# Performance work log

Measured on AMD Instinct MI355X. Metric: run time of the kernel, lower is better.

## Reference

```python
import jax, jax.numpy as jnp
import numpy as np

B, N, C = 16, 1024, 768
NUM_HEADS = 8
HEAD_DIM = C // NUM_HEADS
TEMP_INIT = 0.05
EPS_NORM = 1e-12   # F.normalize eps
EPS_LN = 1e-5      # LayerNorm eps


def setup_inputs() -> dict:
    key = jax.random.key(0)
    ks = jax.random.split(key, 4)
    x = jax.random.normal(ks[0], (B, N, C), dtype=jnp.float32)
    w_qkv = jax.random.normal(ks[1], (3 * C, C), dtype=jnp.float32) * (1.0 / np.sqrt(C))
    w_proj = jax.random.normal(ks[2], (C, C), dtype=jnp.float32) * (1.0 / np.sqrt(C))
    temperature = jnp.ones((NUM_HEADS, 1, 1), dtype=jnp.float32) * TEMP_INIT
    conv_w = jax.random.normal(ks[3], (C, 1, 3, 3), dtype=jnp.float32) * (1.0 / 3.0)
    gamma = jnp.ones((C,), dtype=jnp.float32)
    beta = jnp.zeros((C,), dtype=jnp.float32)
    return {"x": x, "w_qkv": w_qkv, "w_proj": w_proj, "temperature": temperature,
            "conv_w": conv_w, "gamma": gamma, "beta": beta, "H": 32, "W": 32}


def _l2norm_tokens(t):
    # normalize along token dim (axis=-2), matching F.normalize(dim=-2)
    n = jnp.sqrt(jnp.sum(t * t, axis=-2, keepdims=True))
    return t / jnp.maximum(n, EPS_NORM)


def reference(x, w_qkv, w_proj, temperature, conv_w, gamma, beta, H, W):
    b, n, c = x.shape
    h, d = NUM_HEADS, HEAD_DIM
    qkv = (x @ w_qkv.T).reshape(b, n, 3, h, d).transpose(2, 0, 3, 1, 4)  # [3,B,h,N,d]
    q, k, v = qkv[0], qkv[1], qkv[2]
    q = _l2norm_tokens(q)
    k = _l2norm_tokens(k)
    # cross-covariance attention over channels: [B,h,d,d]
    A = jnp.einsum('bhnd,bhne->bhde', q, k) / temperature[None]
    A = jax.nn.softmax(A, axis=-1)
    # v @ A^T : [B,h,N,d]
    x_xca = jnp.einsum('bhne,bhde->bhnd', v, A)
    x_xca = x_xca.transpose(0, 2, 1, 3).reshape(b, n, c)
    x_xca = x_xca @ w_proj.T
    # depthwise 3x3 local propagation
    x_img = x.transpose(0, 2, 1).reshape(b, c, H, W)
    x_local = jax.lax.conv_general_dilated(
        x_img, conv_w, window_strides=(1, 1), padding=((1, 1), (1, 1)),
        dimension_numbers=('NCHW', 'OIHW', 'NCHW'), feature_group_count=c)
    x_local = x_local.reshape(b, c, n).transpose(0, 2, 1)
    y = x_xca + 0.1 * x_local
    mu = jnp.mean(y, axis=-1, keepdims=True)
    var = jnp.mean((y - mu) ** 2, axis=-1, keepdims=True)
    return (y - mu) * jax.lax.rsqrt(var + EPS_LN) * gamma + beta
```

## Files before the change

### kernel.cpp

```cpp
#include <hip/hip_runtime.h>

#define DEVI __device__ __forceinline__

typedef __bf16 bf16x8 __attribute__((ext_vector_type(8)));
typedef float f32x4 __attribute__((ext_vector_type(4)));

DEVI unsigned short f2bf(float f) {
  unsigned u = __builtin_bit_cast(unsigned, f);
  u += 0x7FFFu + ((u >> 16) & 1u);
  return (unsigned short)(u >> 16);
}
DEVI float bf2f(unsigned short s) {
  return __builtin_bit_cast(float, ((unsigned)s) << 16);
}
DEVI f32x4 mfma16(bf16x8 a, bf16x8 b, f32x4 c) {
  return __builtin_amdgcn_mfma_f32_16x16x32_bf16(a, b, c, 0, 0, 0);
}
DEVI void gload16(const void* g, void* l) {
  __builtin_amdgcn_global_load_lds(
      (const __attribute__((address_space(1))) void*)g,
      (__attribute__((address_space(3))) void*)l, 16, 0, 0);
}
template <int ROWB>
DEVI bf16x8 frag_ld(const char* lds, int row, int kb) {
  int off = row * ROWB + (kb ^ ((row & 7) << 4));
  return __builtin_bit_cast(bf16x8, *(const uint4*)(lds + off));
}

__global__ __launch_bounds__(256) void k_cvt2(const float* __restrict__ a,
                                              unsigned short* __restrict__ oa, int n4a,
                                              const float* __restrict__ b,
                                              unsigned short* __restrict__ ob, int n4b) {
  const int tid = threadIdx.x;
  if (blockIdx.x < 2048) {
    const int chunk = (blockIdx.x & 7) * 256 + (blockIdx.x >> 3);
    const int i0 = chunk * 1536;
    for (int i = i0 + tid; i < i0 + 1536; i += 256) {
      float4 f = ((const float4*)a)[i];
      ushort4 o;
      o.x = f2bf(f.x); o.y = f2bf(f.y); o.z = f2bf(f.z); o.w = f2bf(f.w);
      ((ushort4*)oa)[i] = o;
    }
  } else {
    for (int i = (blockIdx.x - 2048) * 256 + tid; i < n4b; i += 256 * 256) {
      float4 f = ((const float4*)b)[i];
      ushort4 o;
      o.x = f2bf(f.x); o.y = f2bf(f.y); o.z = f2bf(f.z); o.w = f2bf(f.w);
      ((ushort4*)ob)[i] = o;
    }
  }
}

template <int MODE>
DEVI void gemm_body(char* lds, const unsigned short* __restrict__ A,
                    const unsigned short* __restrict__ B0,
                    unsigned short* __restrict__ o0, unsigned short* __restrict__ o1,
                    unsigned short* __restrict__ o2) {
  const int tid = threadIdx.x, l = tid & 63, wid = tid >> 6;
  const int wr = wid >> 2, wc = wid & 3;
  const int xg = blockIdx.x;
  const int CPX = MODE ? 64 : 192;
  const int NJT = MODE ? 4 : 12;
  const int li = (xg & 7) * CPX + (xg >> 3);
  const int jt = li % NJT, mt = li / NJT;
  const int m0 = mt * 128, j0 = jt * 192;
  const unsigned short* Bb = MODE ? B0 + (size_t)(m0 >> 10) * 589824 : B0;

  const unsigned short* srcg[4][2];
  int ldso[4][2];
#pragma unroll
  for (int sg = 0; sg < 4; ++sg) {
    const bool isA = (sg == 0) || (sg == 3);
#pragma unroll
    for (int i = 0; i < 2; ++i) {
      int c;
      if (sg == 0)      c = (wid < 4) ? wid : wid + 4;
      else if (sg == 3) c = (wid < 4) ? wid + 4 : wid + 8;
      else if (sg == 1) { int cc = 2 * wid + i; c = (cc >> 2) * 6 + (cc & 3); }
      else              c = (wid >> 1) * 6 + 4 + (wid & 1);
      const int r0 = 8 * c;
      const int r = r0 + (l >> 3);
      const int scol = ((l & 7) ^ (l >> 3)) << 3;
      srcg[sg][i] = (isA ? A + (size_t)(m0 + r) * 768 : Bb + (size_t)(j0 + r) * 768) + scol;
      ldso[sg][i] = (isA ? 0 : 16384) + r0 * 128;
    }
  }
  const int swz = (l & 7) << 4;
  const int uu = (l >> 4) << 4;
  const int c0 = uu ^ swz;
  const int c1 = (64 | uu) ^ swz;
  const int arow = (wr * 64 + (l & 15)) * 128;
  const int brow = 16384 + (wc * 48 + (l & 15)) * 128;

  f32x4 acc[4][3];
#pragma unroll
  for (int i = 0; i < 4; ++i)
#pragma unroll
    for (int j = 0; j < 3; ++j)
#pragma unroll
      for (int e = 0; e < 4; ++e) acc[i][j][e] = 0.f;
  bf16x8 a[2][2], a2[2][2], b01[2][2], b2[2];

#define STAGE1(sg, nxt, ko) \
  gload16(srcg[sg][0] + (ko), lds + (nxt)*40960 + ldso[sg][0])
#define STAGE2(sg, nxt, ko)                                        \
  do {                                                             \
    gload16(srcg[sg][0] + (ko), lds + (nxt)*40960 + ldso[sg][0]);  \
    gload16(srcg[sg][1] + (ko), lds + (nxt)*40960 + ldso[sg][1]);  \
  } while (0)
#define LD128(off) __builtin_bit_cast(bf16x8, *(const uint4*)(cb_ + (off)))

  STAGE1(0, 0, 0); STAGE2(1, 0, 0); STAGE1(2, 0, 0); STAGE1(3, 0, 0);
  asm volatile("s_waitcnt vmcnt(2)" ::: "memory");
  __builtin_amdgcn_s_barrier();

#define KBODY(KT, LASTF)                                                              \
  {                                                                                   \
    const char* cb_ = lds + ((KT) & 1) * 40960;                                       \
    const int nxt = (((KT) & 1) ^ 1);                                                 \
    const int ko = ((KT) + 1) * 64;                                                   \
                           \
    _Pragma("unroll") for (int mf = 0; mf < 2; ++mf) {                                \
      a[mf][0] = LD128(arow + mf * 2048 + c0);                                        \
      a[mf][1] = LD128(arow + mf * 2048 + c1);                                        \
    }                                                                                 \
    _Pragma("unroll") for (int nf = 0; nf < 2; ++nf) {                                \
      b01[nf][0] = LD128(brow + nf * 2048 + c0);                                      \
      b01[nf][1] = LD128(brow + nf * 2048 + c1);                                      \
    }                                                                                 \
    if (!(LASTF)) {                                                                   \
      STAGE1(0, nxt, ko); STAGE2(1, nxt, ko);                                         \
      asm volatile("s_waitcnt vmcnt(3)" ::: "memory");                                \
    } else {                                                                          \
      asm volatile("s_waitcnt vmcnt(0)" ::: "memory");                                \
    }                                                                                 \
    __builtin_amdgcn_s_barrier();                                                     \
    __builtin_amdgcn_s_setprio(1);                                                    \
    _Pragma("unroll") for (int mf = 0; mf < 2; ++mf)                                  \
      _Pragma("unroll") for (int nf = 0; nf < 2; ++nf) {                              \
        acc[mf][nf] = mfma16(a[mf][0], b01[nf][0], acc[mf][nf]);                      \
        acc[mf][nf] = mfma16(a[mf][1], b01[nf][1], acc[mf][nf]);                      \
      }                                                                               \
    __builtin_amdgcn_s_setprio(0);                                                    \
              \
    b2[0] = LD128(brow + 2 * 2048 + c0);                                              \
    b2[1] = LD128(brow + 2 * 2048 + c1);                                              \
    _Pragma("unroll") for (int mf = 0; mf < 2; ++mf) {                                \
      a2[mf][0] = LD128(arow + (mf + 2) * 2048 + c0);                                 \
      a2[mf][1] = LD128(arow + (mf + 2) * 2048 + c1);                                 \
    }                                                                                 \
    if (!(LASTF)) {                                                                   \
      STAGE1(2, nxt, ko); STAGE1(3, nxt, ko);                                         \
      asm volatile("s_waitcnt vmcnt(2)" ::: "memory");                                \
    }                                                                                 \
    __builtin_amdgcn_s_barrier();                                                     \
    __builtin_amdgcn_s_setprio(1);                                                    \
    _Pragma("unroll") for (int mf = 0; mf < 2; ++mf) {                                \
      acc[mf][2] = mfma16(a[mf][0], b2[0], acc[mf][2]);                               \
      acc[mf][2] = mfma16(a[mf][1], b2[1], acc[mf][2]);                               \
    }                                                                                 \
    _Pragma("unroll") for (int mf = 0; mf < 2; ++mf)                                  \
      _Pragma("unroll") for (int nf = 0; nf < 2; ++nf) {                              \
        acc[mf + 2][nf] = mfma16(a2[mf][0], b01[nf][0], acc[mf + 2][nf]);             \
        acc[mf + 2][nf] = mfma16(a2[mf][1], b01[nf][1], acc[mf + 2][nf]);             \
      }                                                                               \
    _Pragma("unroll") for (int mf = 0; mf < 2; ++mf) {                                \
      acc[mf + 2][2] = mfma16(a2[mf][0], b2[0], acc[mf + 2][2]);                      \
      acc[mf + 2][2] = mfma16(a2[mf][1], b2[1], acc[mf + 2][2]);                      \
    }                                                                                 \
    __builtin_amdgcn_s_setprio(0);                                                    \
  }

#pragma unroll 1
  for (int kt = 0; kt < 11; ++kt) KBODY(kt, false);
  KBODY(11, true);
#undef KBODY
#undef STAGE2
#undef STAGE1
#undef LD128

  if constexpr (MODE == 0) {
    const int s = j0 / 768;
    const int jin0 = (j0 % 768) + wc * 48 + (l & 15);
    const int ntok0 = m0 + wr * 64 + ((l >> 4) << 2);
#pragma unroll
    for (int mf = 0; mf < 4; ++mf) {
      const int nt = ntok0 + mf * 16;
      const int bb = nt >> 10, nin = nt & 1023;
#pragma unroll
      for (int nf = 0; nf < 3; ++nf) {
        const int jj = jin0 + nf * 16;
        const int hh = jj / 96, dd = jj % 96;
        if (s == 2) {
          unsigned short* vp = o2 + (size_t)nt * 768 + jj;
#pragma unroll
          for (int rr = 0; rr < 4; ++rr) vp[rr * 768] = f2bf(acc[mf][nf][rr]);
        } else {
          unsigned short* base = (s == 0) ? o0 : o1;
          ushort4 pk;
          pk.x = f2bf(acc[mf][nf][0]); pk.y = f2bf(acc[mf][nf][1]);
          pk.z = f2bf(acc[mf][nf][2]); pk.w = f2bf(acc[mf][nf][3]);
          *(ushort4*)(base + ((size_t)((bb * 8 + hh) * 96 + dd)) * 1024 + nin) = pk;
        }
      }
    }
  } else {
    const int ntok0 = m0 + wr * 64 + ((l >> 4) << 2);
    const int col0 = j0 + wc * 48 + (l & 15);
#pragma unroll
    for (int mf = 0; mf < 4; ++mf)
#pragma unroll
      for (int nf = 0; nf < 3; ++nf) {
        unsigned short* yp = o0 + (size_t)(ntok0 + mf * 16) * 768 + col0 + nf * 16;
#pragma unroll
        for (int rr = 0; rr < 4; ++rr) yp[rr * 768] = f2bf(acc[mf][nf][rr]);
      }
  }
}

__global__ __launch_bounds__(512, 4) void kg0_qkv(const unsigned short* __restrict__ A,
                                                  const unsigned short* __restrict__ B0,
                                                  unsigned short* __restrict__ o0,
                                                  unsigned short* __restrict__ o1,
                                                  unsigned short* __restrict__ o2) {
  __shared__ alignas(16) char lds[81920];
  gemm_body<0>(lds, A, B0, o0, o1, o2);
}
__global__ __launch_bounds__(512, 4) void kg1_proj(const unsigned short* __restrict__ A,
                                                   const unsigned short* __restrict__ B0,
                                                   unsigned short* __restrict__ o0) {
  __shared__ alignas(16) char lds[81920];
  gemm_body<1>(lds, A, B0, o0, nullptr, nullptr);
}

DEVI float ssq8(uint4 u) {
  unsigned a[4] = {u.x, u.y, u.z, u.w};
  float s = 0.f;
#pragma unroll
  for (int i = 0; i < 4; ++i) {
    float lo = __builtin_bit_cast(float, a[i] << 16);
    float hi = __builtin_bit_cast(float, a[i] & 0xFFFF0000u);
    s += lo * lo + hi * hi;
  }
  return s;
}

__global__ __launch_bounds__(256) void k_attn(const unsigned short* __restrict__ qT,
                                              const unsigned short* __restrict__ kT,
                                              const float* __restrict__ temp,
                                              unsigned short* __restrict__ PT) {
  __shared__ alignas(16) char lQK[2][24576];
  __shared__ float lA[96 * 96];
  __shared__ float lrq[96], lrk[96];
  const int blk = blockIdx.x, tid = threadIdx.x, lane = tid & 63, wid = tid >> 6;
  const int idx = blk >> 3;
  const int bb = (blk & 7) * 2 + (idx >> 3);
  const int hh = idx & 7;
  const int bh = bb * 8 + hh;
  const float invt = 1.f / temp[hh];
  const int wr = wid >> 1, wc = wid & 1;
  const unsigned short* qb = qT + (size_t)bh * 96 * 1024;
  const unsigned short* kb = kT + (size_t)bh * 96 * 1024;

  const unsigned short* srcp[6];
  int dsto[6];
#pragma unroll
  for (int i = 0; i < 6; ++i) {
    int cid = wid * 6 + i;
    bool isK = cid >= 12;
    int c = isK ? cid - 12 : cid;
    int p = c * 1024 + lane * 16;
    int r = p >> 7, cb = p & 127;
    int cbs = cb ^ ((r & 7) << 4);
    srcp[i] = (isK ? kb : qb) + (size_t)r * 1024 + (cbs >> 1);
    dsto[i] = (isK ? 12288 : 0) + c * 1024;
  }

#pragma unroll
  for (int i = 0; i < 6; ++i) gload16(srcp[i], lQK[0] + dsto[i]);

  for (int row = wid; row < 192; row += 4) {
    const unsigned short* src = (row < 96) ? qb + (size_t)row * 1024
                                           : kb + (size_t)(row - 96) * 1024;
    const uint4* p = (const uint4*)src + lane * 2;
    float s = ssq8(p[0]) + ssq8(p[1]);
#pragma unroll
    for (int off = 32; off; off >>= 1) s += __shfl_xor(s, off, 64);
    if (lane == 0) {
      float r = 1.f / fmaxf(sqrtf(s), 1e-12f);
      if (row < 96) lrq[row] = r;
      else          lrk[row - 96] = r;
    }
  }

  f32x4 acc[3][3];
#pragma unroll
  for (int i = 0; i < 3; ++i)
#pragma unroll
    for (int j = 0; j < 3; ++j)
#pragma unroll
      for (int e = 0; e < 4; ++e) acc[i][j][e] = 0.f;

  asm volatile("s_waitcnt vmcnt(0)" ::: "memory");
  __builtin_amdgcn_s_barrier();

#pragma unroll 1
  for (int kt = 0; kt < 16; ++kt) {
    const char* bq = lQK[kt & 1];
    if (kt < 15) {
      char* nb = lQK[(kt + 1) & 1];
      const int ko = (kt + 1) * 64;
#pragma unroll
      for (int i = 0; i < 6; ++i) gload16(srcp[i] + ko, nb + dsto[i]);
    }
#pragma unroll
    for (int ks = 0; ks < 2; ++ks) {
      const int kb2 = ks * 64 + ((lane >> 4) << 4);
      bf16x8 af[3], bfv[3];
#pragma unroll
      for (int mb = 0; mb < 3; ++mb) af[mb] = frag_ld<128>(bq, wr * 48 + mb * 16 + (lane & 15), kb2);
#pragma unroll
      for (int nb2 = 0; nb2 < 3; ++nb2) bfv[nb2] = frag_ld<128>(bq + 12288, wc * 48 + nb2 * 16 + (lane & 15), kb2);
#pragma unroll
      for (int mb = 0; mb < 3; ++mb)
#pragma unroll
        for (int nb2 = 0; nb2 < 3; ++nb2) acc[mb][nb2] = mfma16(af[mb], bfv[nb2], acc[mb][nb2]);
    }
    asm volatile("s_waitcnt vmcnt(0)" ::: "memory");
    __builtin_amdgcn_s_barrier();
  }

  const int rb = wr * 48 + ((lane >> 4) << 2);
  const int eb = wc * 48 + (lane & 15);
#pragma unroll
  for (int mb = 0; mb < 3; ++mb)
#pragma unroll
    for (int nb = 0; nb < 3; ++nb) {
      int e = eb + nb * 16;
#pragma unroll
      for (int rr = 0; rr < 4; ++rr) {
        int d = rb + mb * 16 + rr;
        lA[d * 96 + e] = acc[mb][nb][rr] * lrq[d] * lrk[e] * invt;
      }
    }
  __syncthreads();
  for (int d = wid; d < 96; d += 4) {
    float v0 = lA[d * 96 + lane];
    float v1 = (lane < 32) ? lA[d * 96 + 64 + lane] : -3.0e38f;
    float mx = fmaxf(v0, v1);
#pragma unroll
    for (int off = 32; off; off >>= 1) mx = fmaxf(mx, __shfl_xor(mx, off, 64));
    float p0 = __expf(v0 - mx);
    float p1 = (lane < 32) ? __expf(v1 - mx) : 0.f;
    float ssum = p0 + p1;
#pragma unroll
    for (int off = 32; off; off >>= 1) ssum += __shfl_xor(ssum, off, 64);
    float rs = 1.f / ssum;
    PT[((size_t)bh * 96 + lane) * 96 + d] = f2bf(p0 * rs);
    if (lane < 32) PT[((size_t)bh * 96 + 64 + lane) * 96 + d] = f2bf(p1 * rs);
  }
}

__global__ __launch_bounds__(256) void k_prep(const unsigned short* __restrict__ PT,
                                              const float* __restrict__ wproj,
                                              unsigned short* __restrict__ B_all) {
  __shared__ alignas(16) char pl[19968 + 39936];
  unsigned short* lPt = (unsigned short*)pl;
  unsigned short* lW  = (unsigned short*)(pl + 19968);
  unsigned short* tr  = lW;
  const int blk = blockIdx.x;
  const int idx = blk >> 3;
  const int b = (blk & 7) * 2 + (idx >> 5);
  const int h = (idx >> 2) & 7, cq = idx & 3;
  const int tid = threadIdx.x, l = tid & 63, wid = tid >> 6;
  const int wr = wid >> 1, wc = wid & 1;

  const unsigned short* pt = PT + (size_t)(b * 8 + h) * 96 * 96;
  for (int i2 = tid; i2 < 1152; i2 += 256) {
    int r = i2 / 12, ch = i2 % 12;
    *(uint4*)(lPt + r * 104 + ch * 8) = *(const uint4*)(pt + r * 96 + ch * 8);
  }
  for (int i2 = tid; i2 < 4608; i2 += 256) {
    int r = i2 / 24, ch = i2 % 24;
    float4 f = *(const float4*)(wproj + (size_t)(cq * 192 + r) * 768 + h * 96 + ch * 4);
    ushort4 o;
    o.x = f2bf(f.x); o.y = f2bf(f.y); o.z = f2bf(f.z); o.w = f2bf(f.w);
    *(ushort4*)(lW + r * 104 + ch * 4) = o;
  }
  __syncthreads();

  f32x4 acc[3][6];
#pragma unroll
  for (int i = 0; i < 3; ++i)
#pragma unroll
    for (int j = 0; j < 6; ++j)
#pragma unroll
      for (int e = 0; e < 4; ++e) acc[i][j][e] = 0.f;

#pragma unroll
  for (int ks = 0; ks < 3; ++ks) {
    const int kof = ks * 32 + ((l >> 4) << 3);
    bf16x8 af[3], bv[6];
#pragma unroll
    for (int mb = 0; mb < 3; ++mb)
      af[mb] = __builtin_bit_cast(bf16x8, *(const uint4*)(lPt + (wr * 48 + mb * 16 + (l & 15)) * 104 + kof));
#pragma unroll
    for (int nb = 0; nb < 6; ++nb)
      bv[nb] = __builtin_bit_cast(bf16x8, *(const uint4*)(lW + (wc * 96 + nb * 16 + (l & 15)) * 104 + kof));
#pragma unroll
    for (int mb = 0; mb < 3; ++mb)
#pragma unroll
      for (int nb = 0; nb < 6; ++nb) acc[mb][nb] = mfma16(af[mb], bv[nb], acc[mb][nb]);
  }

  __syncthreads();
  const int e0 = wr * 48 + ((l >> 4) << 2);
  const int cl0 = wc * 96 + (l & 15);
#pragma unroll
  for (int mb = 0; mb < 3; ++mb)
#pragma unroll
    for (int nb = 0; nb < 6; ++nb) {
      ushort4 pk;
      pk.x = f2bf(acc[mb][nb][0]); pk.y = f2bf(acc[mb][nb][1]);
      pk.z = f2bf(acc[mb][nb][2]); pk.w = f2bf(acc[mb][nb][3]);
      *(ushort4*)(tr + (cl0 + nb * 16) * 100 + e0 + mb * 16) = pk;
    }
  __syncthreads();
  for (int i2 = tid; i2 < 2304; i2 += 256) {
    int r = i2 / 12, ch = i2 % 12;
    uint4 u = *(const uint4*)(tr + r * 100 + ch * 8);
    *(uint4*)(B_all + ((size_t)(b * 768) + cq * 192 + r) * 768 + h * 96 + ch * 8) = u;
  }
}

__global__ __launch_bounds__(256) void k_final(const unsigned short* __restrict__ yp,
                                               const unsigned short* __restrict__ xb16,
                                               const float* __restrict__ cw,
                                               const float* __restrict__ gamma,
                                               const float* __restrict__ beta,
                                               float* __restrict__ out) {
  const int wid = threadIdx.x >> 6, lane = threadIdx.x & 63;
  const int m = (blockIdx.x & 7) * 2048 + (blockIdx.x >> 3) * 4 + wid;
  const int bb = m >> 10, n = m & 1023, yy = n >> 5, xx = n & 31;
  const unsigned short* xb = xb16 + (size_t)bb * 1024 * 768;

  float yv[3][4];
#pragma unroll
  for (int g = 0; g < 3; ++g) {
    const int c = g * 256 + lane * 4;
    float w36[36];
    const float4* wp = (const float4*)(cw + (size_t)c * 9);
#pragma unroll
    for (int i = 0; i < 9; ++i) *(float4*)(w36 + i * 4) = wp[i];

    float a0 = 0.f, a1 = 0.f, a2 = 0.f, a3 = 0.f;
#pragma unroll
    for (int dy = -1; dy <= 1; ++dy) {
      int ny = yy + dy;
      if ((unsigned)ny < 32u) {
#pragma unroll
        for (int dx = -1; dx <= 1; ++dx) {
          int nx = xx + dx;
          if ((unsigned)nx < 32u) {
            ushort4 v = *(const ushort4*)(xb + (size_t)(ny * 32 + nx) * 768 + c);
            const int j = (dy + 1) * 3 + (dx + 1);
            a0 += w36[0 * 9 + j] * bf2f(v.x);
            a1 += w36[1 * 9 + j] * bf2f(v.y);
            a2 += w36[2 * 9 + j] * bf2f(v.z);
            a3 += w36[3 * 9 + j] * bf2f(v.w);
          }
        }
      }
    }
    ushort4 f = *(const ushort4*)(yp + (size_t)m * 768 + c);
    yv[g][0] = bf2f(f.x) + 0.1f * a0;
    yv[g][1] = bf2f(f.y) + 0.1f * a1;
    yv[g][2] = bf2f(f.z) + 0.1f * a2;
    yv[g][3] = bf2f(f.w) + 0.1f * a3;
  }

  float s1 = 0.f, s2 = 0.f;
#pragma unroll
  for (int g = 0; g < 3; ++g)
#pragma unroll
    for (int e = 0; e < 4; ++e) { s1 += yv[g][e]; s2 += yv[g][e] * yv[g][e]; }
#pragma unroll
  for (int off = 32; off; off >>= 1) {
    s1 += __shfl_xor(s1, off, 64);
    s2 += __shfl_xor(s2, off, 64);
  }
  const float mu = s1 * (1.f / 768.f);
  const float var = s2 * (1.f / 768.f) - mu * mu;
  const float rs = rsqrtf(var + 1e-5f);

#pragma unroll
  for (int g = 0; g < 3; ++g) {
    const int c = g * 256 + lane * 4;
    float4 gm = *(const float4*)(gamma + c);
    float4 bt = *(const float4*)(beta + c);
    float4 o;
    o.x = (yv[g][0] - mu) * rs * gm.x + bt.x;
    o.y = (yv[g][1] - mu) * rs * gm.y + bt.y;
    o.z = (yv[g][2] - mu) * rs * gm.z + bt.z;
    o.w = (yv[g][3] - mu) * rs * gm.w + bt.w;
    *(float4*)(out + (size_t)m * 768 + c) = o;
  }
}

extern "C" void kernel_launch(void* const* d_in, const int* in_sizes, int n_in,
                              void* d_out, int out_size, void* d_ws, size_t ws_size,
                              hipStream_t stream) {
  const float* x     = (const float*)d_in[0];
  const float* wqkv  = (const float*)d_in[1];
  const float* wproj = (const float*)d_in[2];
  const float* temp  = (const float*)d_in[3];
  const float* cw    = (const float*)d_in[4];
  const float* gamma = (const float*)d_in[5];
  const float* beta  = (const float*)d_in[6];
  float* out = (float*)d_out;
  char* ws = (char*)d_ws;

  unsigned short* xb    = (unsigned short*)(ws);
  unsigned short* wqb   = (unsigned short*)(ws + 25165824);
  unsigned short* qT    = (unsigned short*)(ws + 28704768);
  unsigned short* yp    = qT;
  unsigned short* kT    = (unsigned short*)(ws + 53870592);
  unsigned short* B_all = kT;
  unsigned short* vP    = (unsigned short*)(ws + 79036416);
  unsigned short* PT    = (unsigned short*)(ws + 104202240);

  k_cvt2<<<dim3(2304), dim3(256), 0, stream>>>(x, xb, 16384 * 768 / 4,
                                               wqkv, wqb, 2304 * 768 / 4);
  kg0_qkv<<<dim3(1536), dim3(512), 0, stream>>>(xb, wqb, qT, kT, vP);
  k_attn<<<dim3(128), dim3(256), 0, stream>>>(qT, kT, temp, PT);
  k_prep<<<dim3(512), dim3(256), 0, stream>>>(PT, wproj, B_all);
  kg1_proj<<<dim3(512), dim3(512), 0, stream>>>(vP, B_all, yp);
  k_final<<<dim3(4096), dim3(256), 0, stream>>>(yp, xb, cw, gamma, beta, out);
}
```

Measured before the change: 230.2 us.

## Split QKV GEMM into three launches and stage proj epilogue through LDS

The QKV GEMM grid of 1536 blocks is split into three launches of 512 blocks, each with a tile-index offset, so the block-to-tile swizzle uses a stride of 64 inside each chunk. This is likely meant to improve L2 locality of the x and weight tiles. The projection GEMM epilogue now writes the bf16 accumulators into a padded LDS tile and copies the tile to global memory with 16-byte row stores, replacing the scattered 2-byte strided stores. The change adds two kernel launches and one barrier, and it reuses the LDS buffer after the main loop without a barrier before the writes.

```diff
diff --git a/kernel.cpp b/kernel.cpp
--- a/kernel.cpp
+++ b/kernel.cpp
@@ -55,13 +55,12 @@
 DEVI void gemm_body(char* lds, const unsigned short* __restrict__ A,
                     const unsigned short* __restrict__ B0,
                     unsigned short* __restrict__ o0, unsigned short* __restrict__ o1,
-                    unsigned short* __restrict__ o2) {
+                    unsigned short* __restrict__ o2, int li_base) {
   const int tid = threadIdx.x, l = tid & 63, wid = tid >> 6;
   const int wr = wid >> 2, wc = wid & 3;
   const int xg = blockIdx.x;
-  const int CPX = MODE ? 64 : 192;
   const int NJT = MODE ? 4 : 12;
-  const int li = (xg & 7) * CPX + (xg >> 3);
+  const int li = li_base + (xg & 7) * 64 + (xg >> 3);
   const int jt = li % NJT, mt = li / NJT;
   const int m0 = mt * 128, j0 = jt * 192;
   const unsigned short* Bb = MODE ? B0 + (size_t)(m0 >> 10) * 589824 : B0;
@@ -150,7 +149,7 @@
       a2[mf][1] = LD128(arow + (mf + 2) * 2048 + c1);                                 \
     }                                                                                 \
     if (!(LASTF)) {                                                                   \
-      STAGE1(2, nxt, ko); STAGE1(3, nxt, ko);                                         \
+      STAGE1(2, nxt, ko); STAGE1(3, nxt, ko);                                        \
       asm volatile("s_waitcnt vmcnt(2)" ::: "memory");                                \
     }                                                                                 \
     __builtin_amdgcn_s_barrier();                                                     \
@@ -205,16 +204,22 @@
       }
     }
   } else {
-    const int ntok0 = m0 + wr * 64 + ((l >> 4) << 2);
-    const int col0 = j0 + wc * 48 + (l & 15);
+    unsigned short* t = (unsigned short*)lds;
+    const int nl0 = wr * 64 + ((l >> 4) << 2);
+    const int cl0 = wc * 48 + (l & 15);
 #pragma unroll
     for (int mf = 0; mf < 4; ++mf)
 #pragma unroll
-      for (int nf = 0; nf < 3; ++nf) {
-        unsigned short* yp = o0 + (size_t)(ntok0 + mf * 16) * 768 + col0 + nf * 16;
-#pragma unroll
-        for (int rr = 0; rr < 4; ++rr) yp[rr * 768] = f2bf(acc[mf][nf][rr]);
-      }
+      for (int nf = 0; nf < 3; ++nf)
+#pragma unroll
+        for (int rr = 0; rr < 4; ++rr)
+          t[(nl0 + mf * 16 + rr) * 200 + cl0 + nf * 16] = f2bf(acc[mf][nf][rr]);
+    __builtin_amdgcn_s_barrier();
+    for (int i2 = tid; i2 < 3072; i2 += 512) {
+      int r = i2 / 24, ch = i2 % 24;
+      uint4 u = *(const uint4*)(t + r * 200 + ch * 8);
+      *(uint4*)(o0 + (size_t)(m0 + r) * 768 + j0 + ch * 8) = u;
+    }
   }
 }
 
@@ -222,15 +227,16 @@
                                                   const unsigned short* __restrict__ B0,
                                                   unsigned short* __restrict__ o0,
                                                   unsigned short* __restrict__ o1,
-                                                  unsigned short* __restrict__ o2) {
+                                                  unsigned short* __restrict__ o2,
+                                                  int li_base) {
   __shared__ alignas(16) char lds[81920];
-  gemm_body<0>(lds, A, B0, o0, o1, o2);
+  gemm_body<0>(lds, A, B0, o0, o1, o2, li_base);
 }
 __global__ __launch_bounds__(512, 4) void kg1_proj(const unsigned short* __restrict__ A,
                                                    const unsigned short* __restrict__ B0,
                                                    unsigned short* __restrict__ o0) {
   __shared__ alignas(16) char lds[81920];
-  gemm_body<1>(lds, A, B0, o0, nullptr, nullptr);
+  gemm_body<1>(lds, A, B0, o0, nullptr, nullptr, 0);
 }
 
 DEVI float ssq8(uint4 u) {
@@ -531,7 +537,9 @@
 
   k_cvt2<<<dim3(2304), dim3(256), 0, stream>>>(x, xb, 16384 * 768 / 4,
                                                wqkv, wqb, 2304 * 768 / 4);
-  kg0_qkv<<<dim3(1536), dim3(512), 0, stream>>>(xb, wqb, qT, kT, vP);
+  kg0_qkv<<<dim3(512), dim3(512), 0, stream>>>(xb, wqb, qT, kT, vP, 0);
+  kg0_qkv<<<dim3(512), dim3(512), 0, stream>>>(xb, wqb, qT, kT, vP, 512);
+  kg0_qkv<<<dim3(512), dim3(512), 0, stream>>>(xb, wqb, qT, kT, vP, 1024);
   k_attn<<<dim3(128), dim3(256), 0, stream>>>(qT, kT, temp, PT);
   k_prep<<<dim3(512), dim3(256), 0, stream>>>(PT, wproj, B_all);
   kg1_proj<<<dim3(512), dim3(512), 0, stream>>>(vP, B_all, yp);
```

After: 238.7 us. +3.7%, slower.
